# Performance work log

Hardware: AMD Instinct MI355X
Metric: run time of the kernel (lower is better)

The kernel has to match this reference:

```python
import jax, jax.numpy as jnp
import numpy as np

H = 64      # h_dim
E = 64      # embedding_dim
L = 100     # latent_dim
T = 30      # seq_len
DT = 0.03

def _leaky(x):
    return jnp.where(x >= 0, x, 0.01 * x)  # nn.LeakyReLU default slope

def _mlp(h, Ws, bs, Wf, bf):
    # 3 stacked [H,H] LeakyReLU layers + final [L,H] layer, LeakyReLU after EVERY layer (as in source)
    for i in range(Ws.shape[0]):
        h = _leaky(h @ Ws[i].T + bs[i])
    return _leaky(h @ Wf.T + bf)

def _lstm_step(h, c, gates):
    # torch LSTM gate order: i, f, g, o
    i, f, g, o = jnp.split(gates, 4, axis=-1)
    c = jax.nn.sigmoid(f) * c + jax.nn.sigmoid(i) * jnp.tanh(g)
    h = jax.nn.sigmoid(o) * jnp.tanh(c)
    return h, c

def _forward(expert_traj, init_state, eps,
             W_se, b_se,
             W_ih_e, W_hh_e, b_ih_e, b_hh_e,
             mean_Ws, mean_bs, mean_Wf, mean_bf,
             lv_Ws, lv_bs, lv_Wf, lv_bf,
             W_init, b_init,
             W_ih_d, W_hh_d, b_ih_d, b_hh_d,
             W_c, b_c):
    B = expert_traj.shape[0]
    # --- encode: relative positions ---
    rel_xy = jnp.concatenate([expert_traj[:, :1, :2],
                              expert_traj[:, 1:, :2] - expert_traj[:, :-1, :2]], axis=1)
    inp = jnp.concatenate([rel_xy, expert_traj[:, :, 2:]], axis=-1)  # [B,T,4]
    emb = inp @ W_se.T + b_se                                        # [B,T,E]
    x_seq = jnp.swapaxes(emb, 0, 1)                                  # [T,B,E] seq-major
    # precompute input projection for all timesteps in one GEMM
    xp = x_seq @ W_ih_e.T + (b_ih_e + b_hh_e)                        # [T,B,4H]
    h0 = jnp.zeros((B, H), dtype=expert_traj.dtype)
    c0 = jnp.zeros((B, H), dtype=expert_traj.dtype)
    def enc_step(carry, xp_t):
        h, c = carry
        h, c = _lstm_step(h, c, xp_t + h @ W_hh_e.T)
        return (h, c), None
    (hT, _), _ = jax.lax.scan(enc_step, (h0, c0), xp)
    mu = _mlp(hT, mean_Ws, mean_bs, mean_Wf, mean_bf)                # [B,L]
    log_var = _mlp(hT, lv_Ws, lv_bs, lv_Wf, lv_bf)                   # [B,L]
    # --- reparameterize + tanh ---
    z = jnp.tanh(eps * jnp.exp(0.5 * log_var) + mu)
    # --- decode ---
    dh = z @ W_init.T + b_init                                       # [B,H], h0 = c0 = dh
    bias_d = b_ih_d + b_hh_d
    def dec_step(carry, _):
        h, c, prev = carry
        xe = prev @ W_se.T + b_se                                    # spatial embedding of state
        h, c = _lstm_step(h, c, xe @ W_ih_d.T + h @ W_hh_d.T + bias_d)
        ctrl = h @ W_c.T + b_c                                       # [B,2]
        pedal = ctrl[:, 0]
        steer = jnp.clip(ctrl[:, 1], -0.5, 0.5)
        x_t, y_t, psi, v = prev[:, 0], prev[:, 1], prev[:, 2], prev[:, 3]
        v1 = jnp.clip(v + pedal * DT, 0.0, 30.0)
        psi_dot = jnp.clip(v * jnp.tan(steer) / 2.5, -3.14 / 2, 3.14 / 2)
        cur = jnp.stack([x_t + v * jnp.cos(psi) * DT,
                         y_t + v * jnp.sin(psi) * DT,
                         psi + psi_dot * DT,
                         v1], axis=1)
        return (h, c, cur), cur
    _, traj = jax.lax.scan(dec_step, (dh, dh, init_state), None, length=T)
    recons = jnp.swapaxes(traj, 0, 1)                                # [B,T,4]
    return recons, expert_traj, mu, log_var

def setup_inputs() -> dict:
    key = jax.random.key(0)
    ks = jax.random.split(key, 32)
    B = 16384
    s = 0.05
    def p(k, shape):
        return jax.random.normal(k, shape, dtype=jnp.float32) * s
    return {
        "expert_traj": jax.random.normal(ks[0], (B, T, 4), dtype=jnp.float32),
        "init_state": jax.random.normal(ks[1], (B, 4), dtype=jnp.float32),
        "eps": jax.random.normal(ks[2], (B, L), dtype=jnp.float32),
        "W_se": p(ks[3], (E, 4)), "b_se": p(ks[4], (E,)),
        "W_ih_e": p(ks[5], (4 * H, E)), "W_hh_e": p(ks[6], (4 * H, H)),
        "b_ih_e": p(ks[7], (4 * H,)), "b_hh_e": p(ks[8], (4 * H,)),
        "mean_Ws": p(ks[9], (3, H, H)), "mean_bs": p(ks[10], (3, H)),
        "mean_Wf": p(ks[11], (L, H)), "mean_bf": p(ks[12], (L,)),
        "lv_Ws": p(ks[13], (3, H, H)), "lv_bs": p(ks[14], (3, H)),
        "lv_Wf": p(ks[15], (L, H)), "lv_bf": p(ks[16], (L,)),
        "W_init": p(ks[17], (H, L)), "b_init": p(ks[18], (H,)),
        "W_ih_d": p(ks[19], (4 * H, E)), "W_hh_d": p(ks[20], (4 * H, H)),
        "b_ih_d": p(ks[21], (4 * H,)), "b_hh_d": p(ks[22], (4 * H,)),
        "W_c": p(ks[23], (2, H)), "b_c": p(ks[24], (2,)),
    }

def reference(expert_traj, init_state, eps,
              W_se, b_se,
              W_ih_e, W_hh_e, b_ih_e, b_hh_e,
              mean_Ws, mean_bs, mean_Wf, mean_bf,
              lv_Ws, lv_bs, lv_Wf, lv_bf,
              W_init, b_init,
              W_ih_d, W_hh_d, b_ih_d, b_hh_d,
              W_c, b_c):
    return _forward(expert_traj, init_state, eps,
                    W_se, b_se,
                    W_ih_e, W_hh_e, b_ih_e, b_hh_e,
                    mean_Ws, mean_bs, mean_Wf, mean_bf,
                    lv_Ws, lv_bs, lv_Wf, lv_bf,
                    W_init, b_init,
                    W_ih_d, W_hh_d, b_ih_d, b_hh_d,
                    W_c, b_c)
```

## Files before the change

kernel.cpp:

```cpp
#include <hip/hip_runtime.h>

typedef unsigned short u16;
typedef unsigned int u32;
typedef __attribute__((ext_vector_type(8))) short bf16x8;
typedef __attribute__((ext_vector_type(4))) float f32x4;

#define B_TOT 16384
#define RR 16
#define NBLK (B_TOT / RR)
#define TT 30
#define LL 100
#define DTC 0.03f

#define HST 104
#define HBUF_U16 (RR * HST)

#define OFF_H   0
#define OFF_XB  6656
#define OFF_Z   11264
#define OFF_MU  15616
#define OFF_FE  22016
#define OFF_FD  27136
#define OFF_PV  32256
#define OFF_WC  32512
#define SMEM_SZ 33024

__device__ __forceinline__ float bf2f(u16 u) {
    union { u32 i; float f; } v; v.i = ((u32)u) << 16; return v.f;
}
__device__ __forceinline__ u16 f2bf(float f) {
    union { float f; u32 i; } v; v.f = f;
    return (u16)((v.i + 0x7FFFu + ((v.i >> 16) & 1u)) >> 16);
}
__device__ __forceinline__ float rcpf(float x) { return __builtin_amdgcn_rcpf(x); }
__device__ __forceinline__ float tanh_(float x) {
    x = fminf(fmaxf(x, -15.f), 15.f);
    float e = __expf(2.f * x);
    return (e - 1.f) * rcpf(e + 1.f);
}
__device__ __forceinline__ float leaky(float x) { return x >= 0.f ? x : 0.01f * x; }
__device__ __forceinline__ f32x4 mfma16(bf16x8 a, bf16x8 b, f32x4 c) {
    return __builtin_amdgcn_mfma_f32_16x16x32_bf16(a, b, c, 0, 0, 0);
}
__device__ __forceinline__ bf16x8 packw(const float* p) {
    bf16x8 r;
#pragma unroll
    for (int j = 0; j < 8; ++j) r[j] = (short)f2bf(p[j]);
    return r;
}

__global__ __launch_bounds__(256, 4) void vae_lstm_kernel(
    const float* __restrict__ expert, const float* __restrict__ init_state,
    const float* __restrict__ eps,
    const float* __restrict__ W_se, const float* __restrict__ b_se,
    const float* __restrict__ W_ih_e, const float* __restrict__ W_hh_e,
    const float* __restrict__ b_ih_e, const float* __restrict__ b_hh_e,
    const float* __restrict__ mean_Ws, const float* __restrict__ mean_bs,
    const float* __restrict__ mean_Wf, const float* __restrict__ mean_bf,
    const float* __restrict__ lv_Ws, const float* __restrict__ lv_bs,
    const float* __restrict__ lv_Wf, const float* __restrict__ lv_bf,
    const float* __restrict__ W_init, const float* __restrict__ b_init,
    const float* __restrict__ W_ih_d, const float* __restrict__ W_hh_d,
    const float* __restrict__ b_ih_d, const float* __restrict__ b_hh_d,
    const float* __restrict__ W_c, const float* __restrict__ b_c,
    float* __restrict__ out_recons, float* __restrict__ out_expert,
    float* __restrict__ out_mu, float* __restrict__ out_lv)
{
    const int tid = threadIdx.x;
    const int b0g = blockIdx.x * RR;
    const int wv = tid >> 6;
    const int lane = tid & 63;
    const int lcol = lane & 15;
    const int quad = lane >> 4;
    const int jcol = wv * 16 + lcol;

    __shared__ __align__(16) char smem[SMEM_SZ];
    u16* Hbuf   = (u16*)(smem + OFF_H);
    u16* XB0    = (u16*)(smem + OFF_XB);
    u16* XB1    = XB0 + RR * 72;
    u16* zBuf   = (u16*)(smem + OFF_Z);
    float* muBuf = (float*)(smem + OFF_MU);
    u16* inp    = (u16*)(smem + OFF_MU);
    float* fold_e = (float*)(smem + OFF_FE);
    float* fold_d = (float*)(smem + OFF_FD);
    float* sRaw  = (float*)(smem + OFF_XB);
    float* sPrev = (float*)(smem + OFF_PV);
    float* sWc   = (float*)(smem + OFF_WC);

    {
        float me[4] = {0,0,0,0}, md[4] = {0,0,0,0};
        float bea = 0.f, bda = 0.f;
        for (int e = 0; e < 64; ++e) {
            float s0 = W_se[e*4+0], s1 = W_se[e*4+1], s2 = W_se[e*4+2], s3 = W_se[e*4+3];
            float bs = b_se[e];
            float wie = W_ih_e[tid*64+e], wid = W_ih_d[tid*64+e];
            me[0] = fmaf(wie,s0,me[0]); me[1] = fmaf(wie,s1,me[1]);
            me[2] = fmaf(wie,s2,me[2]); me[3] = fmaf(wie,s3,me[3]);
            md[0] = fmaf(wid,s0,md[0]); md[1] = fmaf(wid,s1,md[1]);
            md[2] = fmaf(wid,s2,md[2]); md[3] = fmaf(wid,s3,md[3]);
            bea = fmaf(wie,bs,bea); bda = fmaf(wid,bs,bda);
        }
        float* fp = fold_e + tid*5;
        fp[0]=me[0]; fp[1]=me[1]; fp[2]=me[2]; fp[3]=me[3];
        fp[4] = bea + b_ih_e[tid] + b_hh_e[tid];
        float* fq = fold_d + tid*5;
        fq[0]=md[0]; fq[1]=md[1]; fq[2]=md[2]; fq[3]=md[3];
        fq[4] = bda + b_ih_d[tid] + b_hh_d[tid];
    }

    {
        const int base = b0g * (TT*4);
        for (int idx = tid; idx < RR*TT*4; idx += 256) {
            float v = expert[base + idx];
            sRaw[idx] = v;
            out_expert[base + idx] = v;
        }
        u32* hz = (u32*)Hbuf;
        for (int idx = tid; idx < HBUF_U16; idx += 256) hz[idx] = 0;
        for (int idx = tid; idx < HBUF_U16; idx += 256) hz[HBUF_U16 + idx] = 0;
        __syncthreads();
        for (int idx = tid; idx < RR*TT*4; idx += 256) {
            int q = idx % (TT*4);
            int k = q & 3, t = q >> 2;
            int row = idx / (TT*4);
            float v = sRaw[idx];
            if (k < 2 && t > 0) v -= sRaw[idx - 4];
            u16 hv = f2bf(v);
            inp[idx] = hv;
            if (t == 0) Hbuf[row*HST + 64 + k] = hv;
            if (q == 0) {
                Hbuf[row*HST + 68] = 0x3F80;
                Hbuf[HBUF_U16 + row*HST + 68] = 0x3F80;
            }
        }
        __syncthreads();
    }

    float creg[4] = {0.f, 0.f, 0.f, 0.f};
    bf16x8 bw[4][3];

    auto build_bw = [&](const float* Whh, const float* fold) {
#pragma unroll
        for (int g = 0; g < 4; ++g) {
            const float* wr = Whh + (g*64 + jcol) * 64;
            bw[g][0] = packw(wr + quad*8);
            bw[g][1] = packw(wr + 32 + quad*8);
            bf16x8 t;
#pragma unroll
            for (int j = 0; j < 8; ++j) t[j] = 0;
            if (quad == 0) {
                const float* fp = fold + (g*64 + jcol) * 5;
#pragma unroll
                for (int j = 0; j < 4; ++j) t[j] = (short)f2bf(fp[j]);
                t[4] = (short)f2bf(fp[4]);
            }
            bw[g][2] = t;
        }
    };

    auto lstm_step = [&](const u16* Hc, u16* Hn) {
        bf16x8 a0 = *(const bf16x8*)(Hc + lcol*HST + quad*8);
        bf16x8 a1 = *(const bf16x8*)(Hc + lcol*HST + 32 + quad*8);
        bf16x8 a2 = *(const bf16x8*)(Hc + lcol*HST + 64 + quad*8);
        f32x4 acc[4];
#pragma unroll
        for (int g = 0; g < 4; ++g) {
            f32x4 z = {0.f, 0.f, 0.f, 0.f};
            z = mfma16(a0, bw[g][0], z);
            z = mfma16(a1, bw[g][1], z);
            acc[g] = mfma16(a2, bw[g][2], z);
        }
#pragma unroll
        for (int r = 0; r < 4; ++r) {
            float ig = acc[0][r], fg = acc[1][r], gg = acc[2][r], og = acc[3][r];
            float Ei = __expf(-ig);
            float Ef = __expf(-fg);
            float Eg = __expf(-2.f * gg);
            float P = (1.f + Ei) * (1.f + Eg);
            float Q = 1.f + Ef;
            float num = fmaf(creg[r] * P, Ef, (1.f - Eg) * Q);
            float c = num * rcpf(P * Q);
            creg[r] = c;
            float Ec = __expf(-2.f * c);
            float Eo = __expf(-og);
            float h = (1.f - Ec) * rcpf((1.f + Eo) * (1.f + Ec));
            Hn[(quad*4 + r)*HST + jcol] = f2bf(h);
        }
    };

    build_bw(W_hh_e, fold_e);
    for (int stp = 0; stp < TT; ++stp) {
        const u16* Hc = Hbuf + (stp & 1) * HBUF_U16;
        u16* Hn = Hbuf + ((stp + 1) & 1) * HBUF_U16;
        lstm_step(Hc, Hn);
        if (tid < 64 && stp < TT-1) {
            int row = tid >> 2, k = tid & 3;
            Hn[row*HST + 64 + k] = inp[row*(TT*4) + (stp+1)*4 + k];
        }
        __syncthreads();
    }

    {
        u32* zb = (u32*)zBuf;
        for (int idx = tid; idx < RR*136/2; idx += 256) zb[idx] = 0;
    }

    auto mlp_hidden = [&](const u16* inB, int inStride, u16* outB,
                          const float* Wg, const float* bg) {
        float bv = bg[jcol];
        bf16x8 bb0 = packw(Wg + jcol*64 + quad*8);
        bf16x8 bb1 = packw(Wg + jcol*64 + 32 + quad*8);
        f32x4 acc = {bv, bv, bv, bv};
        bf16x8 a0 = *(const bf16x8*)(inB + lcol*inStride + quad*8);
        bf16x8 a1 = *(const bf16x8*)(inB + lcol*inStride + 32 + quad*8);
        acc = mfma16(a0, bb0, acc);
        acc = mfma16(a1, bb1, acc);
#pragma unroll
        for (int r = 0; r < 4; ++r)
            outB[(quad*4 + r)*72 + jcol] = f2bf(leaky(acc[r]));
        __syncthreads();
    };

    auto mlp_final = [&](const u16* inB, const float* Wg, const float* bg, int mode) {
#pragma unroll
        for (int ni = 0; ni < 2; ++ni) {
            int nt = wv + ni*4;
            if (nt >= 7) continue;
            int n = nt*16 + lcol;
            bool ok = (n < LL);
            float bv = ok ? bg[n] : 0.f;
            bf16x8 bb0, bb1;
            if (ok) {
                bb0 = packw(Wg + n*64 + quad*8);
                bb1 = packw(Wg + n*64 + 32 + quad*8);
            } else {
#pragma unroll
                for (int j = 0; j < 8; ++j) { bb0[j] = 0; bb1[j] = 0; }
            }
            f32x4 acc = {bv, bv, bv, bv};
            bf16x8 a0 = *(const bf16x8*)(inB + lcol*72 + quad*8);
            bf16x8 a1 = *(const bf16x8*)(inB + lcol*72 + 32 + quad*8);
            acc = mfma16(a0, bb0, acc);
            acc = mfma16(a1, bb1, acc);
            if (ok) {
#pragma unroll
                for (int r = 0; r < 4; ++r) {
                    int m = quad*4 + r;
                    float vv = leaky(acc[r]);
                    size_t gi = (size_t)(b0g + m) * LL + n;
                    if (mode == 0) {
                        muBuf[m*LL + n] = vv;
                        out_mu[gi] = vv;
                    } else {
                        out_lv[gi] = vv;
                        float zv = tanh_(fmaf(eps[gi], __expf(0.5f * vv), muBuf[m*LL + n]));
                        zBuf[m*136 + n] = f2bf(zv);
                    }
                }
            }
        }
        __syncthreads();
    };

    mlp_hidden(Hbuf, HST, XB0, mean_Ws, mean_bs);
    mlp_hidden(XB0, 72, XB1, mean_Ws + 4096, mean_bs + 64);
    mlp_hidden(XB1, 72, XB0, mean_Ws + 8192, mean_bs + 128);
    mlp_final(XB0, mean_Wf, mean_bf, 0);
    mlp_hidden(Hbuf, HST, XB0, lv_Ws, lv_bs);
    mlp_hidden(XB0, 72, XB1, lv_Ws + 4096, lv_bs + 64);
    mlp_hidden(XB1, 72, XB0, lv_Ws + 8192, lv_bs + 128);
    mlp_final(XB0, lv_Wf, lv_bf, 1);

    {
        float bv = b_init[jcol];
        bf16x8 bi[4];
#pragma unroll
        for (int kt = 0; kt < 3; ++kt)
            bi[kt] = packw(W_init + jcol*LL + kt*32 + quad*8);
        {
            float f[8];
#pragma unroll
            for (int j = 0; j < 8; ++j) {
                int k = 96 + quad*8 + j;
                f[j] = (k < LL) ? W_init[jcol*LL + k] : 0.f;
            }
            bi[3] = packw(f);
        }
        f32x4 acc = {bv, bv, bv, bv};
#pragma unroll
        for (int kt = 0; kt < 4; ++kt) {
            bf16x8 az = *(const bf16x8*)(zBuf + lcol*136 + kt*32 + quad*8);
            acc = mfma16(az, bi[kt], acc);
        }
#pragma unroll
        for (int r = 0; r < 4; ++r) {
            creg[r] = acc[r];
            Hbuf[(quad*4 + r)*HST + jcol] = f2bf(acc[r]);
        }
        if (tid < RR*4) {
            float v = init_state[b0g*4 + tid];
            sPrev[tid] = v;
            Hbuf[(tid >> 2)*HST + 64 + (tid & 3)] = f2bf(v);
        }
        if (tid < 128) sWc[tid] = W_c[tid];
        __syncthreads();
    }

    build_bw(W_hh_d, fold_d);
    const float bc0 = b_c[0], bc1 = b_c[1];

    for (int stp = 0; stp < TT; ++stp) {
        const u16* Hc = Hbuf + (stp & 1) * HBUF_U16;
        u16* Hn = Hbuf + ((stp + 1) & 1) * HBUF_U16;
        lstm_step(Hc, Hn);
        __syncthreads();
        if (tid < 64) {
            int row = tid >> 2, kq = tid & 3;
            const u16* hr = Hn + row*HST + kq*16;
            bf16x8 h0 = *(const bf16x8*)(hr);
            bf16x8 h1 = *(const bf16x8*)(hr + 8);
            const float4* w0 = (const float4*)(sWc + kq*16);
            const float4* w1 = (const float4*)(sWc + 64 + kq*16);
            float a0 = 0.f, a1 = 0.f;
#pragma unroll
            for (int p = 0; p < 2; ++p) {
                float4 wa = w0[2*p], wb = w0[2*p+1];
                float4 va = w1[2*p], vb = w1[2*p+1];
                bf16x8 hh = p ? h1 : h0;
                float hf[8];
#pragma unroll
                for (int j = 0; j < 8; ++j) hf[j] = bf2f((u16)hh[j]);
                a0 = fmaf(hf[0], wa.x, a0); a0 = fmaf(hf[1], wa.y, a0);
                a0 = fmaf(hf[2], wa.z, a0); a0 = fmaf(hf[3], wa.w, a0);
                a0 = fmaf(hf[4], wb.x, a0); a0 = fmaf(hf[5], wb.y, a0);
                a0 = fmaf(hf[6], wb.z, a0); a0 = fmaf(hf[7], wb.w, a0);
                a1 = fmaf(hf[0], va.x, a1); a1 = fmaf(hf[1], va.y, a1);
                a1 = fmaf(hf[2], va.z, a1); a1 = fmaf(hf[3], va.w, a1);
                a1 = fmaf(hf[4], vb.x, a1); a1 = fmaf(hf[5], vb.y, a1);
                a1 = fmaf(hf[6], vb.z, a1); a1 = fmaf(hf[7], vb.w, a1);
            }
            a0 += __shfl_xor(a0, 1); a1 += __shfl_xor(a1, 1);
            a0 += __shfl_xor(a0, 2); a1 += __shfl_xor(a1, 2);
            if (kq == 0) {
                float pedal = a0 + bc0;
                float steer = fminf(fmaxf(a1 + bc1, -0.5f), 0.5f);
                float4 pv = *(const float4*)(sPrev + row*4);
                float x = pv.x, y = pv.y, psi = pv.z, v = pv.w;
                float v1 = fminf(fmaxf(v + pedal * DTC, 0.f), 30.f);
                float sn, cs;
                __sincosf(psi, &sn, &cs);
                float psid = fminf(fmaxf(v * __tanf(steer) * 0.4f, -1.57f), 1.57f);
                float nx = fmaf(v * cs, DTC, x);
                float ny = fmaf(v * sn, DTC, y);
                float npsi = fmaf(psid, DTC, psi);
                float4 o; o.x = nx; o.y = ny; o.z = npsi; o.w = v1;
                *(float4*)(sPrev + row*4) = o;
                *(float4*)(out_recons + ((size_t)(b0g + row) * TT + stp) * 4) = o;
                u32 lo = (u32)f2bf(nx) | ((u32)f2bf(ny) << 16);
                u32 hi = (u32)f2bf(npsi) | ((u32)f2bf(v1) << 16);
                uint2 pk; pk.x = lo; pk.y = hi;
                *(uint2*)(Hn + row*HST + 64) = pk;
            }
        }
        __syncthreads();
    }
}

extern "C" void kernel_launch(void* const* d_in, const int* in_sizes, int n_in,
                              void* d_out, int out_size, void* d_ws, size_t ws_size,
                              hipStream_t stream) {
    (void)in_sizes; (void)n_in; (void)ws_size; (void)d_ws; (void)out_size;
    const float* expert    = (const float*)d_in[0];
    const float* init_st   = (const float*)d_in[1];
    const float* eps       = (const float*)d_in[2];
    const float* W_se      = (const float*)d_in[3];
    const float* b_se      = (const float*)d_in[4];
    const float* W_ih_e    = (const float*)d_in[5];
    const float* W_hh_e    = (const float*)d_in[6];
    const float* b_ih_e    = (const float*)d_in[7];
    const float* b_hh_e    = (const float*)d_in[8];
    const float* mean_Ws   = (const float*)d_in[9];
    const float* mean_bs   = (const float*)d_in[10];
    const float* mean_Wf   = (const float*)d_in[11];
    const float* mean_bf   = (const float*)d_in[12];
    const float* lv_Ws     = (const float*)d_in[13];
    const float* lv_bs     = (const float*)d_in[14];
    const float* lv_Wf     = (const float*)d_in[15];
    const float* lv_bf     = (const float*)d_in[16];
    const float* W_init    = (const float*)d_in[17];
    const float* b_init    = (const float*)d_in[18];
    const float* W_ih_d    = (const float*)d_in[19];
    const float* W_hh_d    = (const float*)d_in[20];
    const float* b_ih_d    = (const float*)d_in[21];
    const float* b_hh_d    = (const float*)d_in[22];
    const float* W_c       = (const float*)d_in[23];
    const float* b_c       = (const float*)d_in[24];

    float* out = (float*)d_out;
    const size_t n_traj = (size_t)B_TOT * TT * 4;
    const size_t n_lat  = (size_t)B_TOT * LL;
    float* out_recons = out;
    float* out_expert = out + n_traj;
    float* out_mu     = out + 2 * n_traj;
    float* out_lv     = out + 2 * n_traj + n_lat;

    vae_lstm_kernel<<<NBLK, 256, 0, stream>>>(
        expert, init_st, eps, W_se, b_se, W_ih_e, W_hh_e, b_ih_e, b_hh_e,
        mean_Ws, mean_bs, mean_Wf, mean_bf, lv_Ws, lv_bs, lv_Wf, lv_bf,
        W_init, b_init, W_ih_d, W_hh_d, b_ih_d, b_hh_d, W_c, b_c,
        out_recons, out_expert, out_mu, out_lv);
}
```

Before: 245.7 us.

## Precompute bf16 weights and folded projections in a setup kernel, shrink LDS for occupancy

Adds a setup kernel that converts the recurrent, MLP and init weights to bf16 once, folds the input-embedding projection and biases into a padded weight layout, and pre-scales the gate rows by log2(e) so the step can use exp2 directly. The main kernel then loads packed bf16 vectors instead of doing per-block fp32 loads, conversions and the fold loop. LDS shrinks from about 33KB to about 19KB by storing mu as bf16 and reusing buffers, and launch bounds rise to 8 blocks per CU. This costs an extra launch and a workspace round trip, and adds bf16 rounding of mu.

```diff
diff --git a/kernel.cpp b/kernel.cpp
--- a/kernel.cpp
+++ b/kernel.cpp
@@ -11,6 +11,7 @@
 #define TT 30
 #define LL 100
 #define DTC 0.03f
+#define L2E 1.44269504088896f
 
 #define HST 104
 #define HBUF_U16 (RR * HST)
@@ -18,12 +19,17 @@
 #define OFF_H   0
 #define OFF_XB  6656
 #define OFF_Z   11264
-#define OFF_MU  15616
-#define OFF_FE  22016
-#define OFF_FD  27136
-#define OFF_PV  32256
-#define OFF_WC  32512
-#define SMEM_SZ 33024
+#define OFF_U   15616
+#define SMEM_SZ 19456
+
+#define WS_WHHE  0
+#define WS_WHHD  18432
+#define WS_MWS   36864
+#define WS_LWS   49152
+#define WS_MWF   61440
+#define WS_LWF   67840
+#define WS_WINIT 74240
+#define WS_TOTAL 82432
 
 __device__ __forceinline__ float bf2f(u16 u) {
     union { u32 i; float f; } v; v.i = ((u32)u) << 16; return v.f;
@@ -33,6 +39,7 @@
     return (u16)((v.i + 0x7FFFu + ((v.i >> 16) & 1u)) >> 16);
 }
 __device__ __forceinline__ float rcpf(float x) { return __builtin_amdgcn_rcpf(x); }
+__device__ __forceinline__ float ex2(float x) { return __builtin_amdgcn_exp2f(x); }
 __device__ __forceinline__ float tanh_(float x) {
     x = fminf(fmaxf(x, -15.f), 15.f);
     float e = __expf(2.f * x);
@@ -42,27 +49,66 @@
 __device__ __forceinline__ f32x4 mfma16(bf16x8 a, bf16x8 b, f32x4 c) {
     return __builtin_amdgcn_mfma_f32_16x16x32_bf16(a, b, c, 0, 0, 0);
 }
-__device__ __forceinline__ bf16x8 packw(const float* p) {
-    bf16x8 r;
-#pragma unroll
-    for (int j = 0; j < 8; ++j) r[j] = (short)f2bf(p[j]);
-    return r;
-}
-
-__global__ __launch_bounds__(256, 4) void vae_lstm_kernel(
-    const float* __restrict__ expert, const float* __restrict__ init_state,
-    const float* __restrict__ eps,
+
+__global__ void setup_kernel(
     const float* __restrict__ W_se, const float* __restrict__ b_se,
     const float* __restrict__ W_ih_e, const float* __restrict__ W_hh_e,
     const float* __restrict__ b_ih_e, const float* __restrict__ b_hh_e,
-    const float* __restrict__ mean_Ws, const float* __restrict__ mean_bs,
-    const float* __restrict__ mean_Wf, const float* __restrict__ mean_bf,
-    const float* __restrict__ lv_Ws, const float* __restrict__ lv_bs,
-    const float* __restrict__ lv_Wf, const float* __restrict__ lv_bf,
-    const float* __restrict__ W_init, const float* __restrict__ b_init,
     const float* __restrict__ W_ih_d, const float* __restrict__ W_hh_d,
     const float* __restrict__ b_ih_d, const float* __restrict__ b_hh_d,
-    const float* __restrict__ W_c, const float* __restrict__ b_c,
+    const float* __restrict__ mean_Ws, const float* __restrict__ lv_Ws,
+    const float* __restrict__ mean_Wf, const float* __restrict__ lv_Wf,
+    const float* __restrict__ W_init, u16* __restrict__ ws)
+{
+    const int gid = blockIdx.x * 256 + threadIdx.x;
+    const int nth = gridDim.x * 256;
+    for (int i = gid; i < 512; i += nth) {
+        int which = i >> 8, row = i & 255, g = row >> 6;
+        float s = (g == 2) ? 2.f * L2E : L2E;
+        const float* wih = (which ? W_ih_d : W_ih_e) + row * 64;
+        float f0=0,f1=0,f2=0,f3=0,fb=0;
+        for (int e = 0; e < 64; ++e) {
+            float w = wih[e];
+            f0 = fmaf(w, W_se[e*4+0], f0);
+            f1 = fmaf(w, W_se[e*4+1], f1);
+            f2 = fmaf(w, W_se[e*4+2], f2);
+            f3 = fmaf(w, W_se[e*4+3], f3);
+            fb = fmaf(w, b_se[e], fb);
+        }
+        fb += (which ? b_ih_d : b_ih_e)[row] + (which ? b_hh_d : b_hh_e)[row];
+        u16* dst = ws + (which ? WS_WHHD : WS_WHHE) + row * 72 + 64;
+        dst[0]=f2bf(f0*s); dst[1]=f2bf(f1*s); dst[2]=f2bf(f2*s); dst[3]=f2bf(f3*s);
+        dst[4]=f2bf(fb*s); dst[5]=0; dst[6]=0; dst[7]=0;
+    }
+    for (int i = gid; i < 2*16384; i += nth) {
+        int which = i >= 16384;
+        int j = which ? i - 16384 : i;
+        int row = j >> 6, k = j & 63, g = row >> 6;
+        float s = (g == 2) ? 2.f * L2E : L2E;
+        const float* whh = which ? W_hh_d : W_hh_e;
+        ws[(which ? WS_WHHD : WS_WHHE) + row*72 + k] = f2bf(whh[j] * s);
+    }
+    for (int i = gid; i < 12288; i += nth) {
+        ws[WS_MWS + i] = f2bf(mean_Ws[i]);
+        ws[WS_LWS + i] = f2bf(lv_Ws[i]);
+    }
+    for (int i = gid; i < 6400; i += nth) {
+        ws[WS_MWF + i] = f2bf(mean_Wf[i]);
+        ws[WS_LWF + i] = f2bf(lv_Wf[i]);
+    }
+    for (int i = gid; i < 8192; i += nth) {
+        int r = i >> 7, k = i & 127;
+        ws[WS_WINIT + i] = (k < LL) ? f2bf(W_init[r*LL + k]) : (u16)0;
+    }
+}
+
+__global__ __launch_bounds__(256, 8) void vae_lstm_kernel(
+    const float* __restrict__ expert, const float* __restrict__ init_state,
+    const float* __restrict__ eps, const u16* __restrict__ ws,
+    const float* __restrict__ mean_bs, const float* __restrict__ mean_bf,
+    const float* __restrict__ lv_bs, const float* __restrict__ lv_bf,
+    const float* __restrict__ b_init, const float* __restrict__ W_c,
+    const float* __restrict__ b_c,
     float* __restrict__ out_recons, float* __restrict__ out_expert,
     float* __restrict__ out_mu, float* __restrict__ out_lv)
 {
@@ -75,49 +121,25 @@
     const int jcol = wv * 16 + lcol;
 
     __shared__ __align__(16) char smem[SMEM_SZ];
-    u16* Hbuf   = (u16*)(smem + OFF_H);
-    u16* XB0    = (u16*)(smem + OFF_XB);
-    u16* XB1    = XB0 + RR * 72;
-    u16* zBuf   = (u16*)(smem + OFF_Z);
-    float* muBuf = (float*)(smem + OFF_MU);
-    u16* inp    = (u16*)(smem + OFF_MU);
-    float* fold_e = (float*)(smem + OFF_FE);
-    float* fold_d = (float*)(smem + OFF_FD);
+    u16* Hbuf  = (u16*)(smem + OFF_H);
+    u16* XB0   = (u16*)(smem + OFF_XB);
+    u16* XB1   = XB0 + RR * 72;
+    u16* zBuf  = (u16*)(smem + OFF_Z);
+    u16* inp   = (u16*)(smem + OFF_U);
+    u16* muB   = (u16*)(smem + OFF_U);
     float* sRaw  = (float*)(smem + OFF_XB);
-    float* sPrev = (float*)(smem + OFF_PV);
-    float* sWc   = (float*)(smem + OFF_WC);
-
-    {
-        float me[4] = {0,0,0,0}, md[4] = {0,0,0,0};
-        float bea = 0.f, bda = 0.f;
-        for (int e = 0; e < 64; ++e) {
-            float s0 = W_se[e*4+0], s1 = W_se[e*4+1], s2 = W_se[e*4+2], s3 = W_se[e*4+3];
-            float bs = b_se[e];
-            float wie = W_ih_e[tid*64+e], wid = W_ih_d[tid*64+e];
-            me[0] = fmaf(wie,s0,me[0]); me[1] = fmaf(wie,s1,me[1]);
-            me[2] = fmaf(wie,s2,me[2]); me[3] = fmaf(wie,s3,me[3]);
-            md[0] = fmaf(wid,s0,md[0]); md[1] = fmaf(wid,s1,md[1]);
-            md[2] = fmaf(wid,s2,md[2]); md[3] = fmaf(wid,s3,md[3]);
-            bea = fmaf(wie,bs,bea); bda = fmaf(wid,bs,bda);
-        }
-        float* fp = fold_e + tid*5;
-        fp[0]=me[0]; fp[1]=me[1]; fp[2]=me[2]; fp[3]=me[3];
-        fp[4] = bea + b_ih_e[tid] + b_hh_e[tid];
-        float* fq = fold_d + tid*5;
-        fq[0]=md[0]; fq[1]=md[1]; fq[2]=md[2]; fq[3]=md[3];
-        fq[4] = bda + b_ih_d[tid] + b_hh_d[tid];
-    }
+    float* sPrev = (float*)(smem + OFF_XB);
+    float* sWc   = (float*)(smem + OFF_XB + 256);
 
     {
         const int base = b0g * (TT*4);
+        u32* hz = (u32*)Hbuf;
+        for (int idx = tid; idx < HBUF_U16; idx += 256) hz[idx] = 0;
         for (int idx = tid; idx < RR*TT*4; idx += 256) {
             float v = expert[base + idx];
             sRaw[idx] = v;
             out_expert[base + idx] = v;
         }
-        u32* hz = (u32*)Hbuf;
-        for (int idx = tid; idx < HBUF_U16; idx += 256) hz[idx] = 0;
-        for (int idx = tid; idx < HBUF_U16; idx += 256) hz[HBUF_U16 + idx] = 0;
         __syncthreads();
         for (int idx = tid; idx < RR*TT*4; idx += 256) {
             int q = idx % (TT*4);
@@ -139,22 +161,20 @@
     float creg[4] = {0.f, 0.f, 0.f, 0.f};
     bf16x8 bw[4][3];
 
-    auto build_bw = [&](const float* Whh, const float* fold) {
+    auto build_bw = [&](const u16* wsW) {
 #pragma unroll
         for (int g = 0; g < 4; ++g) {
-            const float* wr = Whh + (g*64 + jcol) * 64;
-            bw[g][0] = packw(wr + quad*8);
-            bw[g][1] = packw(wr + 32 + quad*8);
-            bf16x8 t;
-#pragma unroll
-            for (int j = 0; j < 8; ++j) t[j] = 0;
+            const u16* wr = wsW + (g*64 + jcol) * 72;
+            bw[g][0] = *(const bf16x8*)(wr + quad*8);
+            bw[g][1] = *(const bf16x8*)(wr + 32 + quad*8);
             if (quad == 0) {
-                const float* fp = fold + (g*64 + jcol) * 5;
-#pragma unroll
-                for (int j = 0; j < 4; ++j) t[j] = (short)f2bf(fp[j]);
-                t[4] = (short)f2bf(fp[4]);
-            }
-            bw[g][2] = t;
+                bw[g][2] = *(const bf16x8*)(wr + 64);
+            } else {
+                bf16x8 z;
+#pragma unroll
+                for (int j = 0; j < 8; ++j) z[j] = 0;
+                bw[g][2] = z;
+            }
         }
     };
 
@@ -172,23 +192,22 @@
         }
 #pragma unroll
         for (int r = 0; r < 4; ++r) {
-            float ig = acc[0][r], fg = acc[1][r], gg = acc[2][r], og = acc[3][r];
-            float Ei = __expf(-ig);
-            float Ef = __expf(-fg);
-            float Eg = __expf(-2.f * gg);
+            float Ei = ex2(-acc[0][r]);
+            float Ef = ex2(-acc[1][r]);
+            float Eg = ex2(-acc[2][r]);
+            float Eo = ex2(-acc[3][r]);
             float P = (1.f + Ei) * (1.f + Eg);
             float Q = 1.f + Ef;
-            float num = fmaf(creg[r] * P, Ef, (1.f - Eg) * Q);
+            float num = fmaf(creg[r], P, (1.f - Eg) * Q);
             float c = num * rcpf(P * Q);
             creg[r] = c;
-            float Ec = __expf(-2.f * c);
-            float Eo = __expf(-og);
+            float Ec = ex2(-2.f * L2E * c);
             float h = (1.f - Ec) * rcpf((1.f + Eo) * (1.f + Ec));
             Hn[(quad*4 + r)*HST + jcol] = f2bf(h);
         }
     };
 
-    build_bw(W_hh_e, fold_e);
+    build_bw(ws + WS_WHHE);
     for (int stp = 0; stp < TT; ++stp) {
         const u16* Hc = Hbuf + (stp & 1) * HBUF_U16;
         u16* Hn = Hbuf + ((stp + 1) & 1) * HBUF_U16;
@@ -206,10 +225,11 @@
     }
 
     auto mlp_hidden = [&](const u16* inB, int inStride, u16* outB,
-                          const float* Wg, const float* bg) {
+                          const u16* wsW, const float* bg) {
         float bv = bg[jcol];
-        bf16x8 bb0 = packw(Wg + jcol*64 + quad*8);
-        bf16x8 bb1 = packw(Wg + jcol*64 + 32 + quad*8);
+        const u16* wr = wsW + jcol*64;
+        bf16x8 bb0 = *(const bf16x8*)(wr + quad*8);
+        bf16x8 bb1 = *(const bf16x8*)(wr + 32 + quad*8);
         f32x4 acc = {bv, bv, bv, bv};
         bf16x8 a0 = *(const bf16x8*)(inB + lcol*inStride + quad*8);
         bf16x8 a1 = *(const bf16x8*)(inB + lcol*inStride + 32 + quad*8);
@@ -221,7 +241,7 @@
         __syncthreads();
     };
 
-    auto mlp_final = [&](const u16* inB, const float* Wg, const float* bg, int mode) {
+    auto mlp_final = [&](const u16* inB, const u16* wsW, const float* bg, int mode) {
 #pragma unroll
         for (int ni = 0; ni < 2; ++ni) {
             int nt = wv + ni*4;
@@ -231,8 +251,9 @@
             float bv = ok ? bg[n] : 0.f;
             bf16x8 bb0, bb1;
             if (ok) {
-                bb0 = packw(Wg + n*64 + quad*8);
-                bb1 = packw(Wg + n*64 + 32 + quad*8);
+                const u16* wr = wsW + n*64;
+                bb0 = *(const bf16x8*)(wr + quad*8);
+                bb1 = *(const bf16x8*)(wr + 32 + quad*8);
             } else {
 #pragma unroll
                 for (int j = 0; j < 8; ++j) { bb0[j] = 0; bb1[j] = 0; }
@@ -249,11 +270,12 @@
                     float vv = leaky(acc[r]);
                     size_t gi = (size_t)(b0g + m) * LL + n;
                     if (mode == 0) {
-                        muBuf[m*LL + n] = vv;
+                        muB[m*LL + n] = f2bf(vv);
                         out_mu[gi] = vv;
                     } else {
                         out_lv[gi] = vv;
-                        float zv = tanh_(fmaf(eps[gi], __expf(0.5f * vv), muBuf[m*LL + n]));
+                        float mu = bf2f(muB[m*LL + n]);
+                        float zv = tanh_(fmaf(eps[gi], __expf(0.5f * vv), mu));
                         zBuf[m*136 + n] = f2bf(zv);
                     }
                 }
@@ -262,41 +284,31 @@
         __syncthreads();
     };
 
-    mlp_hidden(Hbuf, HST, XB0, mean_Ws, mean_bs);
-    mlp_hidden(XB0, 72, XB1, mean_Ws + 4096, mean_bs + 64);
-    mlp_hidden(XB1, 72, XB0, mean_Ws + 8192, mean_bs + 128);
-    mlp_final(XB0, mean_Wf, mean_bf, 0);
-    mlp_hidden(Hbuf, HST, XB0, lv_Ws, lv_bs);
-    mlp_hidden(XB0, 72, XB1, lv_Ws + 4096, lv_bs + 64);
-    mlp_hidden(XB1, 72, XB0, lv_Ws + 8192, lv_bs + 128);
-    mlp_final(XB0, lv_Wf, lv_bf, 1);
+    mlp_hidden(Hbuf, HST, XB0, ws + WS_MWS, mean_bs);
+    mlp_hidden(XB0, 72, XB1, ws + WS_MWS + 4096, mean_bs + 64);
+    mlp_hidden(XB1, 72, XB0, ws + WS_MWS + 8192, mean_bs + 128);
+    mlp_final(XB0, ws + WS_MWF, mean_bf, 0);
+    mlp_hidden(Hbuf, HST, XB0, ws + WS_LWS, lv_bs);
+    mlp_hidden(XB0, 72, XB1, ws + WS_LWS + 4096, lv_bs + 64);
+    mlp_hidden(XB1, 72, XB0, ws + WS_LWS + 8192, lv_bs + 128);
+    mlp_final(XB0, ws + WS_LWF, lv_bf, 1);
 
     {
         float bv = b_init[jcol];
-        bf16x8 bi[4];
-#pragma unroll
-        for (int kt = 0; kt < 3; ++kt)
-            bi[kt] = packw(W_init + jcol*LL + kt*32 + quad*8);
-        {
-            float f[8];
-#pragma unroll
-            for (int j = 0; j < 8; ++j) {
-                int k = 96 + quad*8 + j;
-                f[j] = (k < LL) ? W_init[jcol*LL + k] : 0.f;
-            }
-            bi[3] = packw(f);
-        }
+        const u16* wr = ws + WS_WINIT + jcol*128;
         f32x4 acc = {bv, bv, bv, bv};
 #pragma unroll
         for (int kt = 0; kt < 4; ++kt) {
             bf16x8 az = *(const bf16x8*)(zBuf + lcol*136 + kt*32 + quad*8);
-            acc = mfma16(az, bi[kt], acc);
+            bf16x8 bi = *(const bf16x8*)(wr + kt*32 + quad*8);
+            acc = mfma16(az, bi, acc);
         }
 #pragma unroll
         for (int r = 0; r < 4; ++r) {
             creg[r] = acc[r];
             Hbuf[(quad*4 + r)*HST + jcol] = f2bf(acc[r]);
         }
+        __syncthreads();
         if (tid < RR*4) {
             float v = init_state[b0g*4 + tid];
             sPrev[tid] = v;
@@ -306,7 +318,7 @@
         __syncthreads();
     }
 
-    build_bw(W_hh_d, fold_d);
+    build_bw(ws + WS_WHHD);
     const float bc0 = b_c[0], bc1 = b_c[1];
 
     for (int stp = 0; stp < TT; ++stp) {
@@ -369,7 +381,7 @@
 extern "C" void kernel_launch(void* const* d_in, const int* in_sizes, int n_in,
                               void* d_out, int out_size, void* d_ws, size_t ws_size,
                               hipStream_t stream) {
-    (void)in_sizes; (void)n_in; (void)ws_size; (void)d_ws; (void)out_size;
+    (void)in_sizes; (void)n_in; (void)ws_size; (void)out_size;
     const float* expert    = (const float*)d_in[0];
     const float* init_st   = (const float*)d_in[1];
     const float* eps       = (const float*)d_in[2];
@@ -404,9 +416,15 @@
     float* out_mu     = out + 2 * n_traj;
     float* out_lv     = out + 2 * n_traj + n_lat;
 
+    u16* ws = (u16*)d_ws;
+
+    setup_kernel<<<64, 256, 0, stream>>>(
+        W_se, b_se, W_ih_e, W_hh_e, b_ih_e, b_hh_e,
+        W_ih_d, W_hh_d, b_ih_d, b_hh_d,
+        mean_Ws, lv_Ws, mean_Wf, lv_Wf, W_init, ws);
+
     vae_lstm_kernel<<<NBLK, 256, 0, stream>>>(
-        expert, init_st, eps, W_se, b_se, W_ih_e, W_hh_e, b_ih_e, b_hh_e,
-        mean_Ws, mean_bs, mean_Wf, mean_bf, lv_Ws, lv_bs, lv_Wf, lv_bf,
-        W_init, b_init, W_ih_d, W_hh_d, b_ih_d, b_hh_d, W_c, b_c,
+        expert, init_st, eps, ws,
+        mean_bs, mean_bf, lv_bs, lv_bf, b_init, W_c, b_c,
         out_recons, out_expert, out_mu, out_lv);
 }
```

Measured after the change: 360.1 us. 46.6% more time.
